# Performance work log

Hardware: AMD Instinct MI355X
Metric: run time of the kernel (lower is better)

## Reference

```python
import jax, jax.numpy as jnp
import numpy as np

N_NODES = 100000
N_EDGES = 1600000


def setup_inputs() -> dict:
    key = jax.random.key(0)
    ks = jax.random.split(key, 8)
    x = jax.random.normal(ks[0], (N_NODES, 128), dtype=jnp.float32)
    edge_index = jax.random.randint(ks[1], (2, N_EDGES), 0, N_NODES, dtype=jnp.int32)
    def glorot(k, fan_in, fan_out):
        s = jnp.sqrt(6.0 / (fan_in + fan_out))
        return jax.random.uniform(k, (fan_in, fan_out), jnp.float32, -s, s)
    return {
        "x": x,
        "edge_index": edge_index,
        "W1": glorot(ks[2], 128, 64), "b1": jnp.zeros((64,), jnp.float32),
        "W2": glorot(ks[3], 64, 64),  "b2": jnp.zeros((64,), jnp.float32),
        "W3": glorot(ks[4], 64, 64),  "b3": jnp.zeros((64,), jnp.float32),
        "W4": glorot(ks[5], 64, 32),  "b4": jnp.zeros((32,), jnp.float32),
    }


def _gcn_norm(edge_index, num_nodes):
    # PyG gcn_norm with added self-loops: deg over destination nodes, sym norm.
    loop = jnp.arange(num_nodes, dtype=edge_index.dtype)
    row = jnp.concatenate([edge_index[0], loop])  # source
    col = jnp.concatenate([edge_index[1], loop])  # destination
    deg = jax.ops.segment_sum(jnp.ones_like(col, dtype=jnp.float32), col,
                              num_segments=num_nodes)
    dinv = jnp.where(deg > 0, jax.lax.rsqrt(deg), 0.0)
    norm = dinv[row] * dinv[col]  # [E + N]
    return row, col, norm


def _gcn_conv(x, W, b, row, col, norm, num_nodes):
    h = x @ W                                   # [N, F_out]
    msg = h[row] * norm[:, None]                # gather + scale  [E+N, F_out]
    out = jax.ops.segment_sum(msg, col, num_segments=num_nodes)  # scatter-add
    return out + b


def reference(x, edge_index, W1, b1, W2, b2, W3, b3, W4, b4):
    n = x.shape[0]
    row, col, norm = _gcn_norm(edge_index, n)
    # dropout is identity in eval mode; ReLU between layers as in forward()
    h = jax.nn.relu(_gcn_conv(x, W1, b1, row, col, norm, n))
    h = jax.nn.relu(_gcn_conv(h, W2, b2, row, col, norm, n))
    h = jax.nn.relu(_gcn_conv(h, W3, b3, row, col, norm, n))
    return _gcn_conv(h, W4, b4, row, col, norm, n)
```

## Files before the change

### kernel.cpp

```cpp
#include <hip/hip_runtime.h>
#include <hip/hip_fp16.h>


#define NBKT 8
#define CAP  262144
#define SUBD 128
#define CAP2 4096

__global__ __launch_bounds__(256) void zero_i32_kernel(int* __restrict__ p, int n) {
    int i = blockIdx.x * blockDim.x + threadIdx.x;
    if (i < n) p[i] = 0;
}

__global__ __launch_bounds__(256) void bin_kernel(const int* __restrict__ row,
                                                  const int* __restrict__ col,
                                                  int* __restrict__ pcnt,
                                                  unsigned* __restrict__ stag,
                                                  int E, int span) {
    __shared__ int scnt[NBKT];
    __shared__ int gbase[NBKT];
    const int tid = threadIdx.x;
    for (int base = blockIdx.x * 1024; base < E; base += gridDim.x * 1024) {
        if (tid < NBKT) scnt[tid] = 0;
        __syncthreads();
        int e0 = base + tid * 4;
        unsigned pk[4]; int pt[4], lp[4];
        if (e0 + 4 <= E) {
            int4 r4 = *(const int4*)(row + e0);
            int4 c4 = *(const int4*)(col + e0);
            int rr[4] = {r4.x, r4.y, r4.z, r4.w};
            int cc[4] = {c4.x, c4.y, c4.z, c4.w};
#pragma unroll
            for (int u = 0; u < 4; ++u) {
                int p = cc[u] / span;
                pt[u] = p;
                pk[u] = ((unsigned)rr[u] << 14) | (unsigned)(cc[u] - p * span);
                lp[u] = atomicAdd(&scnt[p], 1);
            }
        } else {
#pragma unroll
            for (int u = 0; u < 4; ++u) {
                int e = e0 + u;
                if (e < E) {
                    int r = row[e], c = col[e];
                    int p = c / span;
                    pt[u] = p;
                    pk[u] = ((unsigned)r << 14) | (unsigned)(c - p * span);
                    lp[u] = atomicAdd(&scnt[p], 1);
                } else pt[u] = -1;
            }
        }
        __syncthreads();
        if (tid < NBKT) gbase[tid] = atomicAdd(&pcnt[tid], scnt[tid]);
        __syncthreads();
#pragma unroll
        for (int u = 0; u < 4; ++u) {
            if (e0 + u < E) {
                stag[(size_t)pt[u] * CAP + (unsigned)(gbase[pt[u]] + lp[u])] = pk[u];
            }
        }
        __syncthreads();
    }
}

__global__ __launch_bounds__(256) void bin2_kernel(const unsigned* __restrict__ stag1,
                                                   const int* __restrict__ pcnt,
                                                   int* __restrict__ pcnt2,
                                                   unsigned* __restrict__ stag2,
                                                   int nsb) {
    __shared__ int scnt[128];
    __shared__ int gbase[128];
    const int part = blockIdx.x & 7;
    const int n = min(pcnt[part], CAP);
    const unsigned* s = stag1 + (size_t)part * CAP;
    const int t0 = (blockIdx.x >> 3) * 4096;
    if (t0 >= n) return;
    const int tn = min(4096, n - t0);
    const int tid = threadIdx.x;

    for (int i = tid; i < nsb; i += 256) scnt[i] = 0;
    __syncthreads();
    for (int i = tid; i < tn; i += 256) {
        unsigned v = s[t0 + i];
        atomicAdd(&scnt[(v & 0x3FFF) >> 7], 1);
    }
    __syncthreads();
    for (int i = tid; i < nsb; i += 256) {
        gbase[i] = atomicAdd(&pcnt2[part * nsb + i], scnt[i]);
        scnt[i] = 0;
    }
    __syncthreads();
    for (int i = tid; i < tn; i += 256) {
        unsigned v = s[t0 + i];
        int cl = v & 0x3FFF;
        int sb = cl >> 7;
        int lp = atomicAdd(&scnt[sb], 1);
        int pos = min(gbase[sb] + lp, CAP2 - 1);
        stag2[(size_t)(part * nsb + sb) * CAP2 + pos] = ((v >> 14) << 7) | (unsigned)(cl & 127);
    }
}

__global__ __launch_bounds__(1024) void scan_small_kernel(const int* __restrict__ src,
                                                          int* __restrict__ dst, int n) {
    __shared__ int s[1024];
    int tid = threadIdx.x;
    int v = (tid < n) ? src[tid] : 0;
    s[tid] = v;
    __syncthreads();
    for (int off = 1; off < 1024; off <<= 1) {
        int t = (tid >= off) ? s[tid - off] : 0;
        __syncthreads();
        s[tid] += t;
        __syncthreads();
    }
    if (tid < n) dst[tid] = s[tid] - v;
}

__global__ __launch_bounds__(256) void sort_sub_kernel(const unsigned* __restrict__ stag2,
                                                       const int* __restrict__ pcnt2,
                                                       const int* __restrict__ sbase,
                                                       int* __restrict__ offs2,
                                                       int* __restrict__ eidx,
                                                       int span, int nsb, int E) {
    __shared__ int cnt[1024];
    __shared__ int tsum[256];
    __shared__ int lout[CAP2];
    const int part = blockIdx.x & 7;
    const int sb   = blockIdx.x >> 3;
    if (sb >= nsb) return;
    const int sbg  = part * nsb + sb;
    const int n    = min(pcnt2[sbg], CAP2);
    const unsigned* s = stag2 + (size_t)sbg * CAP2;
    const int base = sbase[sbg];
    const int c0   = part * span + sb * SUBD;
    const int dd   = min(SUBD, span - sb * SUBD);
    const int tid  = threadIdx.x;

    for (int i = tid; i < 1024; i += 256) cnt[i] = 0;
    __syncthreads();
    for (int i = tid; i < n; i += 256) {
        unsigned v = s[i];
        int r = v >> 7;
        atomicAdd(&cnt[((v & 127) << 3) | (r / span)], 1);
    }
    __syncthreads();
    int a0 = cnt[tid * 4], a1 = cnt[tid * 4 + 1], a2 = cnt[tid * 4 + 2], a3 = cnt[tid * 4 + 3];
    int tot = a0 + a1 + a2 + a3;
    tsum[tid] = tot;
    __syncthreads();
    for (int off = 1; off < 256; off <<= 1) {
        int t = (tid >= off) ? tsum[tid - off] : 0;
        __syncthreads();
        tsum[tid] += t;
        __syncthreads();
    }
    int pre = tsum[tid] - tot;
    cnt[tid * 4]     = pre;
    cnt[tid * 4 + 1] = pre + a0;
    cnt[tid * 4 + 2] = pre + a0 + a1;
    cnt[tid * 4 + 3] = pre + a0 + a1 + a2;
    __syncthreads();
    for (int k = tid; k < dd * 8; k += 256) offs2[(size_t)c0 * 8 + k] = base + cnt[k];
    if (part == NBKT - 1 && sb == nsb - 1 && tid == 0) offs2[(size_t)(c0 + dd) * 8] = base + n;
    __syncthreads();
    for (int i = tid; i < n; i += 256) {
        unsigned v = s[i];
        int r = v >> 7;
        int p = atomicAdd(&cnt[((v & 127) << 3) | (r / span)], 1);
        lout[p] = r;
    }
    __syncthreads();
    for (int i = tid; i < n; i += 256) eidx[base + i] = lout[i];
}

__global__ __launch_bounds__(256) void dinv2_kernel(const int* __restrict__ offs2,
                                                    float* __restrict__ dinv, int N) {
    int i = blockIdx.x * blockDim.x + threadIdx.x;
    if (i < N) {
        int deg = offs2[i * NBKT + NBKT] - offs2[i * NBKT];
        dinv[i] = rsqrtf((float)deg + 1.0f);
    }
}

template <int F_IN, int F_OUT, bool RELU>
__global__ __launch_bounds__(256, 4) void gemm_tile_kernel(const float* __restrict__ in,
                                                           const float* __restrict__ W,
                                                           const float* __restrict__ dinv,
                                                           ushort* __restrict__ outh, int N) {
    constexpr int TC   = F_OUT / 4;
    constexpr int TR   = 256 / TC;
    constexpr int ROWS = TR * 4;
    constexpr int NKB  = F_IN / 64;
    __shared__ float sIn[ROWS][68];
    __shared__ float sW[64][F_OUT];

    const int tc = threadIdx.x % TC;
    const int tr = threadIdx.x / TC;
    const int r0 = blockIdx.x * ROWS;

    float acc[4][4] = {};

#pragma unroll
    for (int kb = 0; kb < NKB; ++kb) {
        if (kb) __syncthreads();
        for (int idx = threadIdx.x; idx < ROWS * 16; idx += 256) {
            int rr = idx / 16, c4 = (idx % 16) * 4;
            int gr = min(r0 + rr, N - 1);
            float4 v = *(const float4*)&in[(size_t)gr * F_IN + kb * 64 + c4];
            if (RELU) {
                v.x = fmaxf(v.x, 0.f); v.y = fmaxf(v.y, 0.f);
                v.z = fmaxf(v.z, 0.f); v.w = fmaxf(v.w, 0.f);
            }
            *(float4*)&sIn[rr][c4] = v;
        }
        for (int idx = threadIdx.x; idx < 64 * F_OUT / 4; idx += 256) {
            int kr = idx / (F_OUT / 4), c4 = (idx % (F_OUT / 4)) * 4;
            *(float4*)&sW[kr][c4] = *(const float4*)&W[(size_t)(kb * 64 + kr) * F_OUT + c4];
        }
        __syncthreads();
#pragma unroll 2
        for (int kk = 0; kk < 64; kk += 4) {
            float4 iv[4], wv[4];
#pragma unroll
            for (int i = 0; i < 4; ++i) iv[i] = *(const float4*)&sIn[tr * 4 + i][kk];
#pragma unroll
            for (int q = 0; q < 4; ++q) wv[q] = *(const float4*)&sW[kk + q][tc * 4];
#pragma unroll
            for (int i = 0; i < 4; ++i) {
                const float ik[4] = {iv[i].x, iv[i].y, iv[i].z, iv[i].w};
#pragma unroll
                for (int q = 0; q < 4; ++q) {
                    acc[i][0] = fmaf(ik[q], wv[q].x, acc[i][0]);
                    acc[i][1] = fmaf(ik[q], wv[q].y, acc[i][1]);
                    acc[i][2] = fmaf(ik[q], wv[q].z, acc[i][2]);
                    acc[i][3] = fmaf(ik[q], wv[q].w, acc[i][3]);
                }
            }
        }
    }
#pragma unroll
    for (int i = 0; i < 4; ++i) {
        int r = r0 + tr * 4 + i;
        if (r < N) {
            float d = dinv[r];
            ushort4 v;
            v.x = __half_as_ushort(__float2half(acc[i][0] * d));
            v.y = __half_as_ushort(__float2half(acc[i][1] * d));
            v.z = __half_as_ushort(__float2half(acc[i][2] * d));
            v.w = __half_as_ushort(__float2half(acc[i][3] * d));
            *(ushort4*)&outh[(size_t)r * F_OUT + tc * 4] = v;
        }
    }
}

__device__ inline void h8acc(float* acc, uint4 u) {
    const __half2* p = (const __half2*)&u;
#pragma unroll
    for (int i = 0; i < 4; ++i) {
        float2 f = __half22float2(p[i]);
        acc[2 * i]     += f.x;
        acc[2 * i + 1] += f.y;
    }
}

template <int F>
__global__ __launch_bounds__(256) void agg_half_kernel(const ushort* __restrict__ h,
                                                       const int* __restrict__ offs2,
                                                       const int* __restrict__ eidx,
                                                       const float* __restrict__ dinv,
                                                       const float* __restrict__ b,
                                                       float* __restrict__ out, int N) {
    constexpr int L = F / 8;
    int tid = blockIdx.x * 256 + threadIdx.x;
    int seg = tid / L;
    int jw  = tid % L;
    if (seg >= N) return;
    const uint4* hv = (const uint4*)h;

    int k = offs2[(size_t)seg * NBKT];
    const int e = offs2[(size_t)seg * NBKT + NBKT];

    float a0[8] = {}, a1[8] = {};
    for (; k + 4 <= e; k += 4) {
        int r0 = eidx[k], r1 = eidx[k + 1], r2 = eidx[k + 2], r3 = eidx[k + 3];
        uint4 u0 = hv[(size_t)r0 * L + jw];
        uint4 u1 = hv[(size_t)r1 * L + jw];
        uint4 u2 = hv[(size_t)r2 * L + jw];
        uint4 u3 = hv[(size_t)r3 * L + jw];
        h8acc(a0, u0); h8acc(a1, u1); h8acc(a0, u2); h8acc(a1, u3);
    }
    if (k + 2 <= e) {
        int r0 = eidx[k], r1 = eidx[k + 1];
        uint4 u0 = hv[(size_t)r0 * L + jw];
        uint4 u1 = hv[(size_t)r1 * L + jw];
        h8acc(a0, u0); h8acc(a1, u1);
        k += 2;
    }
    if (k < e) h8acc(a0, hv[(size_t)eidx[k] * L + jw]);

    h8acc(a0, hv[(size_t)seg * L + jw]);
#pragma unroll
    for (int i = 0; i < 8; ++i) a0[i] += a1[i];

    float  d  = dinv[seg];
    float4 b0 = *(const float4*)&b[jw * 8];
    float4 b1 = *(const float4*)&b[jw * 8 + 4];
    float4 o0 = {b0.x + d * a0[0], b0.y + d * a0[1], b0.z + d * a0[2], b0.w + d * a0[3]};
    float4 o1 = {b1.x + d * a0[4], b1.y + d * a0[5], b1.z + d * a0[6], b1.w + d * a0[7]};
    *(float4*)&out[(size_t)seg * F + jw * 8]     = o0;
    *(float4*)&out[(size_t)seg * F + jw * 8 + 4] = o1;
}

extern "C" void kernel_launch(void* const* d_in, const int* in_sizes, int n_in,
                              void* d_out, int out_size, void* d_ws, size_t ws_size,
                              hipStream_t stream) {
    const float* x  = (const float*)d_in[0];
    const int*   ei = (const int*)d_in[1];
    const float* W1 = (const float*)d_in[2];
    const float* b1 = (const float*)d_in[3];
    const float* W2 = (const float*)d_in[4];
    const float* b2 = (const float*)d_in[5];
    const float* W3 = (const float*)d_in[6];
    const float* b3 = (const float*)d_in[7];
    const float* W4 = (const float*)d_in[8];
    const float* b4 = (const float*)d_in[9];

    const int N = in_sizes[0] / 128;
    const int E = in_sizes[1] / 2;
    const int* row = ei;
    const int* col = ei + E;
    const int n2   = N * NBKT;
    const int span = (N + NBKT - 1) / NBKT;
    const int nsb  = (span + SUBD - 1) / SUBD;

    char* w = (char*)d_ws;
    int*      offs2 = (int*)w;               w += (size_t)(n2 + 4) * 4;
    float*    dinv  = (float*)w;             w += (size_t)N * 4;
    int*      eidx  = (int*)w;               w += (size_t)E * 4;
    unsigned* stag1 = (unsigned*)w;          w += (size_t)NBKT * CAP * 4;
    float*    X     = (float*)w;             w += (size_t)N * 64 * 4;
    ushort*   H     = (ushort*)w;
    unsigned* stag2 = (unsigned*)X;
    int*      pcnt2 = (int*)(stag2 + (size_t)NBKT * nsb * CAP2);
    int*      pcnt  = pcnt2 + NBKT * nsb;
    int*      sbase = pcnt + NBKT;
    float*    out   = (float*)d_out;

    const int T  = 256;
    const int NB = (N + T - 1) / T;

    zero_i32_kernel<<<(NBKT * nsb + NBKT + T - 1) / T, T, 0, stream>>>(pcnt2, NBKT * nsb + NBKT);
    bin_kernel<<<1024, T, 0, stream>>>(row, col, pcnt, stag1, E, span);
    bin2_kernel<<<8 * (CAP / 4096), T, 0, stream>>>(stag1, pcnt, pcnt2, stag2, nsb);
    scan_small_kernel<<<1, 1024, 0, stream>>>(pcnt2, sbase, NBKT * nsb);
    sort_sub_kernel<<<8 * nsb, T, 0, stream>>>(stag2, pcnt2, sbase, offs2, eidx, span, nsb, E);
    dinv2_kernel<<<NB, T, 0, stream>>>(offs2, dinv, N);

    const int g64 = (N + 63) / 64;
    const int g32 = (N + 127) / 128;
    const int a64 = (N * 8 + T - 1) / T;
    const int a32 = (N * 4 + T - 1) / T;

    gemm_tile_kernel<128, 64, false><<<g64, T, 0, stream>>>(x, W1, dinv, H, N);
    agg_half_kernel<64><<<a64, T, 0, stream>>>(H, offs2, eidx, dinv, b1, X, N);
    gemm_tile_kernel<64, 64, true><<<g64, T, 0, stream>>>(X, W2, dinv, H, N);
    agg_half_kernel<64><<<a64, T, 0, stream>>>(H, offs2, eidx, dinv, b2, X, N);
    gemm_tile_kernel<64, 64, true><<<g64, T, 0, stream>>>(X, W3, dinv, H, N);
    agg_half_kernel<64><<<a64, T, 0, stream>>>(H, offs2, eidx, dinv, b3, X, N);
    gemm_tile_kernel<64, 32, true><<<g32, T, 0, stream>>>(X, W4, dinv, H, N);
    agg_half_kernel<32><<<a32, T, 0, stream>>>(H, offs2, eidx, dinv, b4, out, N);
}
```

Measured before the change: 312.9 us.

## Fuse neighbor aggregation with next-layer GEMM into one kernel per layer

Adds a kernel that gathers fp16 neighbor features for a tile of rows, applies bias, ReLU and normalization into shared memory, then multiplies by the next layer's weight and writes fp16 output. This removes the fp32 intermediate X buffer round trip and three kernel launches between layers. In exchange the gather phase runs at coarser per-block granularity with more shared memory per block, which can reduce occupancy and load balance for skewed degrees.

```diff
diff --git a/kernel.cpp b/kernel.cpp
--- a/kernel.cpp
+++ b/kernel.cpp
@@ -263,6 +263,111 @@
     }
 }
 
+template <int F_OUT>
+__global__ __launch_bounds__(256, 4) void fused_agg_gemm_kernel(
+    const ushort* __restrict__ hin,
+    const int* __restrict__ offs2,
+    const int* __restrict__ eidx,
+    const float* __restrict__ dinv,
+    const float* __restrict__ bias,
+    const float* __restrict__ W,
+    ushort* __restrict__ hout, int N) {
+    constexpr int TC   = F_OUT / 4;
+    constexpr int TR   = 256 / TC;
+    constexpr int ROWS = TR * 4;
+    constexpr int L    = 8;
+    __shared__ float sIn[ROWS][68];
+    __shared__ float sW[64][F_OUT];
+
+    const int tid = threadIdx.x;
+    const int r0  = blockIdx.x * ROWS;
+    const uint4* hv = (const uint4*)hin;
+
+    const int jw  = tid & 7;
+    const int grp = tid >> 3;
+    float bj[8];
+#pragma unroll
+    for (int i = 0; i < 8; ++i) bj[i] = bias[jw * 8 + i];
+
+#pragma unroll
+    for (int pass = 0; pass < ROWS / 32; ++pass) {
+        int rl  = pass * 32 + grp;
+        int seg = r0 + rl;
+        if (seg < N) {
+            float a0[8] = {}, a1[8] = {};
+            int k = offs2[(size_t)seg * NBKT];
+            const int e = offs2[(size_t)seg * NBKT + NBKT];
+            for (; k + 4 <= e; k += 4) {
+                int s0 = eidx[k], s1 = eidx[k + 1], s2 = eidx[k + 2], s3 = eidx[k + 3];
+                uint4 u0 = hv[(size_t)s0 * L + jw];
+                uint4 u1 = hv[(size_t)s1 * L + jw];
+                uint4 u2 = hv[(size_t)s2 * L + jw];
+                uint4 u3 = hv[(size_t)s3 * L + jw];
+                h8acc(a0, u0); h8acc(a1, u1); h8acc(a0, u2); h8acc(a1, u3);
+            }
+            if (k + 2 <= e) {
+                int s0 = eidx[k], s1 = eidx[k + 1];
+                uint4 u0 = hv[(size_t)s0 * L + jw];
+                uint4 u1 = hv[(size_t)s1 * L + jw];
+                h8acc(a0, u0); h8acc(a1, u1);
+                k += 2;
+            }
+            if (k < e) h8acc(a0, hv[(size_t)eidx[k] * L + jw]);
+            h8acc(a0, hv[(size_t)seg * L + jw]);
+            float d = dinv[seg];
+#pragma unroll
+            for (int i = 0; i < 8; ++i) {
+                float v = bj[i] + d * (a0[i] + a1[i]);
+                sIn[rl][jw * 8 + i] = fmaxf(v, 0.0f);
+            }
+        } else {
+#pragma unroll
+            for (int i = 0; i < 8; ++i) sIn[rl][jw * 8 + i] = 0.0f;
+        }
+    }
+    for (int idx = tid; idx < 64 * F_OUT / 4; idx += 256) {
+        int kr = idx / (F_OUT / 4), c4 = (idx % (F_OUT / 4)) * 4;
+        *(float4*)&sW[kr][c4] = *(const float4*)&W[(size_t)kr * F_OUT + c4];
+    }
+    __syncthreads();
+
+    const int tc = tid % TC;
+    const int tr = tid / TC;
+    float acc[4][4] = {};
+#pragma unroll 2
+    for (int kk = 0; kk < 64; kk += 4) {
+        float4 iv[4], wv[4];
+#pragma unroll
+        for (int i = 0; i < 4; ++i) iv[i] = *(const float4*)&sIn[tr * 4 + i][kk];
+#pragma unroll
+        for (int q = 0; q < 4; ++q) wv[q] = *(const float4*)&sW[kk + q][tc * 4];
+#pragma unroll
+        for (int i = 0; i < 4; ++i) {
+            const float ik[4] = {iv[i].x, iv[i].y, iv[i].z, iv[i].w};
+#pragma unroll
+            for (int q = 0; q < 4; ++q) {
+                acc[i][0] = fmaf(ik[q], wv[q].x, acc[i][0]);
+                acc[i][1] = fmaf(ik[q], wv[q].y, acc[i][1]);
+                acc[i][2] = fmaf(ik[q], wv[q].z, acc[i][2]);
+                acc[i][3] = fmaf(ik[q], wv[q].w, acc[i][3]);
+            }
+        }
+    }
+#pragma unroll
+    for (int i = 0; i < 4; ++i) {
+        int r = r0 + tr * 4 + i;
+        if (r < N) {
+            float d = dinv[r];
+            ushort4 v;
+            v.x = __half_as_ushort(__float2half(acc[i][0] * d));
+            v.y = __half_as_ushort(__float2half(acc[i][1] * d));
+            v.z = __half_as_ushort(__float2half(acc[i][2] * d));
+            v.w = __half_as_ushort(__float2half(acc[i][3] * d));
+            *(ushort4*)&hout[(size_t)r * F_OUT + tc * 4] = v;
+        }
+    }
+}
+
 template <int F>
 __global__ __launch_bounds__(256) void agg_half_kernel(const ushort* __restrict__ h,
                                                        const int* __restrict__ offs2,
@@ -338,9 +443,9 @@
     float*    dinv  = (float*)w;             w += (size_t)N * 4;
     int*      eidx  = (int*)w;               w += (size_t)E * 4;
     unsigned* stag1 = (unsigned*)w;          w += (size_t)NBKT * CAP * 4;
-    float*    X     = (float*)w;             w += (size_t)N * 64 * 4;
-    ushort*   H     = (ushort*)w;
-    unsigned* stag2 = (unsigned*)X;
+    ushort*   HA    = (ushort*)w;            w += (size_t)N * 64 * 2;
+    ushort*   HB    = (ushort*)w;
+    unsigned* stag2 = (unsigned*)HA;
     int*      pcnt2 = (int*)(stag2 + (size_t)NBKT * nsb * CAP2);
     int*      pcnt  = pcnt2 + NBKT * nsb;
     int*      sbase = pcnt + NBKT;
@@ -357,16 +462,13 @@
     dinv2_kernel<<<NB, T, 0, stream>>>(offs2, dinv, N);
 
     const int g64 = (N + 63) / 64;
-    const int g32 = (N + 127) / 128;
-    const int a64 = (N * 8 + T - 1) / T;
+    const int f64 = (N + 63) / 64;
+    const int f32b = (N + 127) / 128;
     const int a32 = (N * 4 + T - 1) / T;
 
-    gemm_tile_kernel<128, 64, false><<<g64, T, 0, stream>>>(x, W1, dinv, H, N);
-    agg_half_kernel<64><<<a64, T, 0, stream>>>(H, offs2, eidx, dinv, b1, X, N);
-    gemm_tile_kernel<64, 64, true><<<g64, T, 0, stream>>>(X, W2, dinv, H, N);
-    agg_half_kernel<64><<<a64, T, 0, stream>>>(H, offs2, eidx, dinv, b2, X, N);
-    gemm_tile_kernel<64, 64, true><<<g64, T, 0, stream>>>(X, W3, dinv, H, N);
-    agg_half_kernel<64><<<a64, T, 0, stream>>>(H, offs2, eidx, dinv, b3, X, N);
-    gemm_tile_kernel<64, 32, true><<<g32, T, 0, stream>>>(X, W4, dinv, H, N);
-    agg_half_kernel<32><<<a32, T, 0, stream>>>(H, offs2, eidx, dinv, b4, out, N);
-}
+    gemm_tile_kernel<128, 64, false><<<g64, T, 0, stream>>>(x, W1, dinv, HA, N);
+    fused_agg_gemm_kernel<64><<<f64, T, 0, stream>>>(HA, offs2, eidx, dinv, b1, W2, HB, N);
+    fused_agg_gemm_kernel<64><<<f64, T, 0, stream>>>(HB, offs2, eidx, dinv, b2, W3, HA, N);
+    fused_agg_gemm_kernel<32><<<f32b, T, 0, stream>>>(HA, offs2, eidx, dinv, b3, W4, HB, N);
+    agg_half_kernel<32><<<a32, T, 0, stream>>>(HB, offs2, eidx, dinv, b4, out, N);
+}
```

After: 301.5 us. 3.7% less time.
